# Optimization experiments

Hardware: AMD Instinct MI355X
Metric: run time of the kernel (lower is better)

Reference implementation:

```python
import jax, jax.numpy as jnp
import numpy as np

B, S, HID, NH, CACHE = 2, 1024, 1024, 16, 4096
HD = HID // NH
HOT = max(4, CACHE // 4)
COLD = CACHE - HOT
COMP = HID // 2
EPS = 1e-5


def setup_inputs() -> dict:
    key = jax.random.key(0)
    ks = jax.random.split(key, 16)
    std = 0.02
    inp = {
        'inputs': jax.random.normal(ks[0], (B, S, HID), jnp.float32),
        'hot_keys': std * jax.random.normal(ks[1], (HOT, HID), jnp.float32),
        'hot_values': std * jax.random.normal(ks[2], (HOT, HID), jnp.float32),
        'hot_age': jnp.zeros((HOT,), jnp.float32),
        'hot_access': jnp.zeros((HOT,), jnp.float32),
        'cold_keys': std * jax.random.normal(ks[3], (COLD, HID), jnp.float32),
        'cold_values': std * jax.random.normal(ks[4], (COLD, HID), jnp.float32),
        'cold_age': jnp.zeros((COLD,), jnp.float32),
        'cold_access': jnp.zeros((COLD,), jnp.float32),
        # linear weights stored [in, out] (y = x @ W + b)
        'Wq': std * jax.random.normal(ks[5], (HID, HID), jnp.float32),
        'bq': jnp.zeros((HID,), jnp.float32),
        'Wk': std * jax.random.normal(ks[6], (HID, HID), jnp.float32),
        'bk': jnp.zeros((HID,), jnp.float32),
        'Wv': std * jax.random.normal(ks[7], (HID, HID), jnp.float32),
        'bv': jnp.zeros((HID,), jnp.float32),
        'Wo': std * jax.random.normal(ks[8], (HID, HID), jnp.float32),
        'bo': jnp.zeros((HID,), jnp.float32),
        'Wc': (1.0 / np.sqrt(HID)) * jax.random.normal(ks[9], (HID, COMP), jnp.float32),
        'bc': jnp.zeros((COMP,), jnp.float32),
        'Wd': (1.0 / np.sqrt(COMP)) * jax.random.normal(ks[10], (COMP, HID), jnp.float32),
        'bd': jnp.zeros((HID,), jnp.float32),
        'gamma': jnp.ones((HID,), jnp.float32),
        'beta': jnp.zeros((HID,), jnp.float32),
    }
    return inp


def _cache_level(q, cache_k, v_flat, age, access, Wk, bk, Wo, bo):
    # q: [B, NH, S, HD]; cache_k/v_flat: [C, HID]
    C = cache_k.shape[0]
    k = (cache_k @ Wk + bk).reshape(C, NH, HD)
    v = v_flat.reshape(C, NH, HD)
    scores = jnp.einsum('bhsd,chd->bhsc', q, k) / np.sqrt(HD)
    scores = scores + (-0.1 * age + 0.05 * access)  # broadcast over [B,H,S,C]
    attn = jax.nn.softmax(scores, axis=-1)
    out = jnp.einsum('bhsc,chd->bhsd', attn, v)
    out = out.transpose(0, 2, 1, 3).reshape(q.shape[0], q.shape[2], HID)
    return out @ Wo + bo


def reference(inputs, hot_keys, hot_values, hot_age, hot_access,
              cold_keys, cold_values, cold_age, cold_access,
              Wq, bq, Wk, bk, Wv, bv, Wo, bo, Wc, bc, Wd, bd, gamma, beta):
    q = (inputs @ Wq + bq).reshape(B, S, NH, HD).transpose(0, 2, 1, 3)
    # hot tier: values through value_net
    hot_v = hot_values @ Wv + bv
    hot_out = _cache_level(q, hot_keys, hot_v, hot_age, hot_access, Wk, bk, Wo, bo)
    # cold tier: values through compressor -> decompressor
    cold_v = (cold_values @ Wc + bc) @ Wd + bd
    cold_out = _cache_level(q, cold_keys, cold_v, cold_age, cold_access, Wk, bk, Wo, bo)
    x = hot_out + cold_out
    mu = jnp.mean(x, axis=-1, keepdims=True)
    var = jnp.mean(jnp.square(x - mu), axis=-1, keepdims=True)
    return (x - mu) / jnp.sqrt(var + EPS) * gamma + beta
```

## Files before the change

kernel.cpp:

```cpp
#include <hip/hip_runtime.h>

#define BBATCH 2
#define SS   1024
#define HID  1024
#define NH   16
#define HD   64
#define HOT  1024
#define COLD 3072
#define COMP 512

typedef __attribute__((ext_vector_type(8))) short s8v;
typedef __attribute__((ext_vector_type(4))) float f4v;
typedef unsigned short u16;
typedef unsigned int   u32;

__device__ __forceinline__ float b2f(u16 u){ return __uint_as_float(((u32)u)<<16); }
__device__ __forceinline__ u16 f2b(float f){
  u32 u = __float_as_uint(f);
  u += 0x7FFF + ((u>>16)&1);
  return (u16)(u>>16);
}
__device__ __forceinline__ u32 pk2r(u32 a, u32 b){
  return __builtin_amdgcn_perm(b + 0x8000u, a + 0x8000u, 0x07060302u);
}
__device__ __forceinline__ float ldsc(const void* p, int i, int isf32){
  return isf32 ? ((const float*)p)[i] : b2f(((const u16*)p)[i]);
}
__device__ __forceinline__ void gl16(const u16* g, u16* l){
  __builtin_amdgcn_global_load_lds(
      (const __attribute__((address_space(1))) u32*)g,
      (__attribute__((address_space(3))) u32*)l, 16, 0, 0);
}

__global__ void detect_kernel(const u32* __restrict__ gamma_raw, u32* __restrict__ flag){
  if (threadIdx.x == 0) flag[0] = (gamma_raw[0] == 0x3F800000u) ? 1u : 0u;
}

__global__ __launch_bounds__(256) void bias_kernel(
    const void* __restrict__ h_age, const void* __restrict__ h_acc,
    const void* __restrict__ c_age, const void* __restrict__ c_acc,
    float* __restrict__ BiasH, float* __restrict__ BiasC, const u32* __restrict__ flag)
{
  const int f = (int)flag[0];
  const int i = blockIdx.x * 256 + threadIdx.x;
  if (i < HOT) BiasH[i] = -0.1f * ldsc(h_age, i, f) + 0.05f * ldsc(h_acc, i, f);
  const int j = i - HOT;
  if (j >= 0 && j < COLD) BiasC[j] = -0.1f * ldsc(c_age, j, f) + 0.05f * ldsc(c_acc, j, f);
}

struct CDesc { const void* S; u16* D; int tile0, pad; };
struct CBatch { CDesc d[5]; int nd; };

__global__ __launch_bounds__(256) void convert_multi(CBatch cb, const u32* __restrict__ flag)
{
  int di = 0;
  for (int i = 1; i < cb.nd; i++) if ((int)blockIdx.x >= cb.d[i].tile0) di = i;
  const CDesc g = cb.d[di];
  const int f = (int)flag[0];
  const size_t e0 = (size_t)(blockIdx.x - g.tile0) * 2048 + (size_t)threadIdx.x * 8;
  if (f) {
    const float* s = (const float*)g.S + e0;
    const uint4 x = *(const uint4*)s, y = *(const uint4*)(s + 4);
    *(uint4*)(g.D + e0) =
      (uint4){ pk2r(x.x,x.y), pk2r(x.z,x.w), pk2r(y.x,y.y), pk2r(y.z,y.w) };
  } else {
    *(uint4*)(g.D + e0) = *(const uint4*)((const u16*)g.S + e0);
  }
}

struct TDesc { const void* S; u16* D; int R, C, cshift, tile0; };
struct TBatch { TDesc d[6]; int nd; };

__global__ __launch_bounds__(256) void transpose_kernel(TBatch tb, const u32* __restrict__ flag)
{
  __shared__ __align__(16) u16 Tt[64][72];
  int di = 0;
  for (int i = 1; i < tb.nd; i++) if ((int)blockIdx.x >= tb.d[i].tile0) di = i;
  const TDesc g = tb.d[di];
  const int local = blockIdx.x - g.tile0;
  const int ty = local >> g.cshift;
  const int tx = local & ((1 << g.cshift) - 1);
  const int r0 = ty * 64, c0 = tx * 64;
  const int f = (int)flag[0];
  const int t = threadIdx.x;
  const int sr = t >> 2, sc = (t & 3) * 16;

  union { uint4 q[2]; u16 h[16]; } u;
  if (f) {
    const float* s = (const float*)g.S + (size_t)(r0 + sr) * g.C + c0 + sc;
    const uint4 a = *(const uint4*)s,     b = *(const uint4*)(s + 4);
    const uint4 c = *(const uint4*)(s + 8), d2 = *(const uint4*)(s + 12);
    u.q[0] = (uint4){ pk2r(a.x,a.y), pk2r(a.z,a.w), pk2r(b.x,b.y), pk2r(b.z,b.w) };
    u.q[1] = (uint4){ pk2r(c.x,c.y), pk2r(c.z,c.w), pk2r(d2.x,d2.y), pk2r(d2.z,d2.w) };
  } else {
    const u16* s = (const u16*)g.S + (size_t)(r0 + sr) * g.C + c0 + sc;
    u.q[0] = *(const uint4*)s;  u.q[1] = *(const uint4*)(s + 8);
  }
  #pragma unroll
  for (int i = 0; i < 16; i++) Tt[sc + i][sr] = u.h[i];
  __syncthreads();

  const int dc = t >> 2, dr = (t & 3) * 16;
  const uint4 o0 = *(const uint4*)&Tt[dc][dr];
  const uint4 o1 = *(const uint4*)&Tt[dc][dr + 8];
  u16* dp = g.D + (size_t)(c0 + dc) * g.R + r0 + dr;
  *(uint4*)dp = o0;  *(uint4*)(dp + 8) = o1;
}

#define BM 128
#define BN 64
#define BK 32
#define GSW(row, blk) (((row) << 5) + ((((blk) ^ (((row) >> 1) & 3))) << 3))

struct GemmDesc {
  const void* A; const u16* BT; const void* bias; u16* C;
  int aflag, bcol0, M, N, K, nxlog, tile0, ctrans;
  float bias_scale;
};
struct GemmBatch { GemmDesc d[6]; int nd; };

__global__ __launch_bounds__(256) void gemm_multi(GemmBatch bat, const u32* __restrict__ flag)
{
  __shared__ __align__(16) u16 As[BM * BK];
  __shared__ __align__(16) u16 Bs[BN * BK];

  int di = 0;
  for (int i = 1; i < bat.nd; i++) if ((int)blockIdx.x >= bat.d[i].tile0) di = i;
  const GemmDesc g = bat.d[di];
  const int local = blockIdx.x - g.tile0;
  const int ty = local >> g.nxlog;
  const int tx = local - (ty << g.nxlog);
  const int m0 = ty * BM, n0 = tx * BN;

  const int f  = (int)flag[0];
  const int af = g.aflag ? f : 0;

  const int tid  = threadIdx.x;
  const int lane = tid & 63, wave = tid >> 6;
  const int quad = lane >> 4, l15 = lane & 15;
  const int wy = wave >> 1, wx = wave & 1;

  f4v acc[4][2];
  #pragma unroll
  for (int i = 0; i < 4; i++)
    #pragma unroll
    for (int j = 0; j < 2; j++) acc[i][j] = (f4v){0.f,0.f,0.f,0.f};

  const int lrow = lane >> 2, lpos = lane & 3;
  const int arow0 = wave * 32 + lrow, arow1 = arow0 + 16;
  const int brow  = wave * 16 + lrow;
  const u16* gA0 = (const u16*)g.A + (size_t)(m0 + arow0) * g.K + ((lpos ^ ((arow0 >> 1) & 3)) << 3);
  const u16* gA1 = (const u16*)g.A + (size_t)(m0 + arow1) * g.K + ((lpos ^ ((arow1 >> 1) & 3)) << 3);
  const u16* gB0 = g.BT + (size_t)(g.bcol0 + n0 + brow) * g.K + ((lpos ^ ((brow >> 1) & 3)) << 3);
  u16* lA0 = &As[wave * 1024];
  u16* lA1 = &As[wave * 1024 + 512];
  u16* lB0 = &Bs[wave * 512];

  const int ar = tid >> 1, ac = (tid & 1) * 16;
  const int sAr = (ar >> 1) & 3, b0i = (tid & 1) * 2;
  uint4 a0, a1, a2, a3;
  auto load_Aregs = [&](int kk) {
    const float* s = (const float*)g.A + (size_t)(m0 + ar) * g.K + kk + ac;
    a0 = *(const uint4*)s;       a1 = *(const uint4*)(s + 4);
    a2 = *(const uint4*)(s + 8); a3 = *(const uint4*)(s + 12);
  };
  if (af) load_Aregs(0);

  for (int k0 = 0; k0 < g.K; k0 += BK) {
    __syncthreads();
    if (af) {
      *(uint4*)&As[(ar << 5) + (((b0i    ) ^ sAr) << 3)] =
        (uint4){ pk2r(a0.x,a0.y), pk2r(a0.z,a0.w), pk2r(a1.x,a1.y), pk2r(a1.z,a1.w) };
      *(uint4*)&As[(ar << 5) + (((b0i + 1) ^ sAr) << 3)] =
        (uint4){ pk2r(a2.x,a2.y), pk2r(a2.z,a2.w), pk2r(a3.x,a3.y), pk2r(a3.z,a3.w) };
    } else {
      gl16(gA0 + k0, lA0);
      gl16(gA1 + k0, lA1);
    }
    gl16(gB0 + k0, lB0);
    __syncthreads();

    if (af && k0 + BK < g.K) load_Aregs(k0 + BK);

    s8v afr[4], bfr[2];
    #pragma unroll
    for (int i = 0; i < 4; i++) {
      const int rr = wy * 64 + i * 16 + l15;
      afr[i] = *(const s8v*)&As[GSW(rr, quad)];
    }
    #pragma unroll
    for (int j = 0; j < 2; j++) {
      const int rb = wx * 32 + j * 16 + l15;
      bfr[j] = *(const s8v*)&Bs[GSW(rb, quad)];
    }

    #pragma unroll
    for (int j = 0; j < 2; j++)
      #pragma unroll
      for (int i = 0; i < 4; i++)
        acc[i][j] = __builtin_amdgcn_mfma_f32_16x16x32_bf16(afr[i], bfr[j], acc[i][j], 0, 0, 0);
  }

  if (g.ctrans) {
    #pragma unroll
    for (int j = 0; j < 2; j++) {
      const int col = n0 + wx * 32 + j * 16 + l15;
      const float bv = ldsc(g.bias, g.bcol0 + col, f) * g.bias_scale;
      #pragma unroll
      for (int i = 0; i < 4; i++) {
        const int row = m0 + wy * 64 + i * 16 + quad * 4;
        u16 t4[4];
        #pragma unroll
        for (int r = 0; r < 4; r++) t4[r] = f2b(acc[i][j][r] + bv);
        *(uint2*)&g.C[(size_t)col * g.M + row] = *(uint2*)t4;
      }
    }
  } else {
    #pragma unroll
    for (int j = 0; j < 2; j++) {
      const int col = n0 + wx * 32 + j * 16 + l15;
      const float bv = ldsc(g.bias, g.bcol0 + col, f) * g.bias_scale;
      #pragma unroll
      for (int i = 0; i < 4; i++) {
        const int row = m0 + wy * 64 + i * 16 + quad * 4;
        #pragma unroll
        for (int r = 0; r < 4; r++)
          g.C[(size_t)(row + r) * g.N + col] = f2b(acc[i][j][r] + bv);
      }
    }
  }
}

#define KV(row, blk) (((row) << 6) + ((((blk) ^ ((row) & 7))) << 3))

__global__ __launch_bounds__(256) void attn_kernel(
    const u16* __restrict__ Q,
    const u16* __restrict__ KHg, const u16* __restrict__ VHT,
    const u16* __restrict__ KCg, const u16* __restrict__ VCT,
    const float* __restrict__ BiasH, const float* __restrict__ BiasC,
    float* __restrict__ HotOut, float* __restrict__ ColdNum3, float* __restrict__ ColdZ3,
    int NG, int glog)
{
  __shared__ __align__(16) u16 Ks[64 * 64];
  __shared__ __align__(16) u16 Vs[64 * 64];

  const int tid  = threadIdx.x;
  const int lane = tid & 63, wave = tid >> 6;
  const int quad = lane >> 4, l15 = lane & 15;

  const int bx    = blockIdx.x;
  const int slice = bx & 3;
  const int sblk  = (bx >> 2) & 7;
  const int h     = (bx >> 5) & ((1 << glog) - 1);
  const int b     = bx >> (5 + glog);

  const int rowbase = b * SS + sblk * 128;
  const int hoff  = h * HD;
  const int myrow = wave * 32;

  const bool hot = (slice == 0);
  const u16*  Kt   = hot ? KHg : KCg;
  const u16*  Vt   = hot ? VHT : VCT;
  const float* Bias = hot ? BiasH : BiasC;
  const int   e0  = hot ? 0 : (slice - 1) * 1024;
  const int   ldv = hot ? HOT : COLD;

  const u16* qp = Q + (size_t)(rowbase + myrow + l15) * NG + hoff + quad * 8;
  const s8v aq0 = *(const s8v*)qp;
  const s8v aq1 = *(const s8v*)(qp + 32);
  const u16* qp1 = qp + (size_t)16 * NG;
  const s8v aq2 = *(const s8v*)qp1;
  const s8v aq3 = *(const s8v*)(qp1 + 32);

  const int rk = tid >> 2, cb2 = (tid & 3) * 2, sk = (tid & 3) * 16;
  const u16* kbase = Kt + (size_t)(e0 + rk) * NG + hoff + sk;
  const u16* vbase = Vt + (size_t)(hoff + rk) * ldv + e0 + sk;
  uint4 kr0 = *(const uint4*)kbase, kr1 = *(const uint4*)(kbase + 8);
  uint4 vr0 = *(const uint4*)vbase, vr1 = *(const uint4*)(vbase + 8);

  u16* kw0 = &Ks[KV(rk, cb2)];     u16* kw1 = &Ks[KV(rk, cb2 + 1)];
  u16* vw0 = &Vs[KV(rk, cb2)];     u16* vw1 = &Vs[KV(rk, cb2 + 1)];

  f4v o0[4], o1[4];
  #pragma unroll
  for (int j = 0; j < 4; j++) { o0[j] = (f4v){0.f,0.f,0.f,0.f}; o1[j] = (f4v){0.f,0.f,0.f,0.f}; }
  float zs0 = 0.f, zs1 = 0.f;

  for (int c0 = 0; c0 < 1024; c0 += 64) {
    __syncthreads();
    *(uint4*)kw0 = kr0;  *(uint4*)kw1 = kr1;
    *(uint4*)vw0 = vr0;  *(uint4*)vw1 = vr1;
    __syncthreads();
    if (c0 + 64 < 1024) {
      const u16* kn = kbase + (size_t)(c0 + 64) * NG;
      const u16* vn = vbase + (c0 + 64);
      kr0 = *(const uint4*)kn;  kr1 = *(const uint4*)(kn + 8);
      vr0 = *(const uint4*)vn;  vr1 = *(const uint4*)(vn + 8);
    }

    #pragma unroll
    for (int h2 = 0; h2 < 2; h2++) {
      const s8v ka0 = *(const s8v*)&Ks[KV(h2 * 32 + l15, quad)];
      const s8v ka1 = *(const s8v*)&Ks[KV(h2 * 32 + l15, 4 + quad)];
      const s8v kb0 = *(const s8v*)&Ks[KV(h2 * 32 + 16 + l15, quad)];
      const s8v kb1 = *(const s8v*)&Ks[KV(h2 * 32 + 16 + l15, 4 + quad)];

      const int cg0 = e0 + c0 + h2 * 32 + quad * 4;
      const float4 bi0 = *(const float4*)&Bias[cg0];
      const float4 bi1 = *(const float4*)&Bias[cg0 + 16];

      union { u32 w[4]; s8v v; } ap0, ap1;
      {
        f4v s0 = (f4v){0.f,0.f,0.f,0.f}, s1 = (f4v){0.f,0.f,0.f,0.f};
        s0 = __builtin_amdgcn_mfma_f32_16x16x32_bf16(ka0, aq0, s0, 0, 0, 0);
        s0 = __builtin_amdgcn_mfma_f32_16x16x32_bf16(ka1, aq1, s0, 0, 0, 0);
        s1 = __builtin_amdgcn_mfma_f32_16x16x32_bf16(kb0, aq0, s1, 0, 0, 0);
        s1 = __builtin_amdgcn_mfma_f32_16x16x32_bf16(kb1, aq1, s1, 0, 0, 0);
        float p0[4], p1[4];
        p0[0] = __expf(fminf(s0[0] * 0.125f + bi0.x, 30.f));
        p0[1] = __expf(fminf(s0[1] * 0.125f + bi0.y, 30.f));
        p0[2] = __expf(fminf(s0[2] * 0.125f + bi0.z, 30.f));
        p0[3] = __expf(fminf(s0[3] * 0.125f + bi0.w, 30.f));
        p1[0] = __expf(fminf(s1[0] * 0.125f + bi1.x, 30.f));
        p1[1] = __expf(fminf(s1[1] * 0.125f + bi1.y, 30.f));
        p1[2] = __expf(fminf(s1[2] * 0.125f + bi1.z, 30.f));
        p1[3] = __expf(fminf(s1[3] * 0.125f + bi1.w, 30.f));
        zs0 += p0[0] + p0[1] + p0[2] + p0[3] + p1[0] + p1[1] + p1[2] + p1[3];
        const u32 W0 = pk2r(__float_as_uint(p0[0]), __float_as_uint(p0[1]));
        const u32 W1 = pk2r(__float_as_uint(p0[2]), __float_as_uint(p0[3]));
        const u32 W2 = pk2r(__float_as_uint(p1[0]), __float_as_uint(p1[1]));
        const u32 W3 = pk2r(__float_as_uint(p1[2]), __float_as_uint(p1[3]));
        #pragma unroll
        for (int t = 0; t < 4; t++) {
          const int srcl = (((quad << 1) + (t >> 1)) & 3) * 16 + l15;
          const u32 lo = __shfl((t & 1) ? W1 : W0, srcl, 64);
          const u32 hi = __shfl((t & 1) ? W3 : W2, srcl, 64);
          ap0.w[t] = (quad >= 2) ? hi : lo;
        }
      }
      {
        f4v s0 = (f4v){0.f,0.f,0.f,0.f}, s1 = (f4v){0.f,0.f,0.f,0.f};
        s0 = __builtin_amdgcn_mfma_f32_16x16x32_bf16(ka0, aq2, s0, 0, 0, 0);
        s0 = __builtin_amdgcn_mfma_f32_16x16x32_bf16(ka1, aq3, s0, 0, 0, 0);
        s1 = __builtin_amdgcn_mfma_f32_16x16x32_bf16(kb0, aq2, s1, 0, 0, 0);
        s1 = __builtin_amdgcn_mfma_f32_16x16x32_bf16(kb1, aq3, s1, 0, 0, 0);
        float p0[4], p1[4];
        p0[0] = __expf(fminf(s0[0] * 0.125f + bi0.x, 30.f));
        p0[1] = __expf(fminf(s0[1] * 0.125f + bi0.y, 30.f));
        p0[2] = __expf(fminf(s0[2] * 0.125f + bi0.z, 30.f));
        p0[3] = __expf(fminf(s0[3] * 0.125f + bi0.w, 30.f));
        p1[0] = __expf(fminf(s1[0] * 0.125f + bi1.x, 30.f));
        p1[1] = __expf(fminf(s1[1] * 0.125f + bi1.y, 30.f));
        p1[2] = __expf(fminf(s1[2] * 0.125f + bi1.z, 30.f));
        p1[3] = __expf(fminf(s1[3] * 0.125f + bi1.w, 30.f));
        zs1 += p0[0] + p0[1] + p0[2] + p0[3] + p1[0] + p1[1] + p1[2] + p1[3];
        const u32 W0 = pk2r(__float_as_uint(p0[0]), __float_as_uint(p0[1]));
        const u32 W1 = pk2r(__float_as_uint(p0[2]), __float_as_uint(p0[3]));
        const u32 W2 = pk2r(__float_as_uint(p1[0]), __float_as_uint(p1[1]));
        const u32 W3 = pk2r(__float_as_uint(p1[2]), __float_as_uint(p1[3]));
        #pragma unroll
        for (int t = 0; t < 4; t++) {
          const int srcl = (((quad << 1) + (t >> 1)) & 3) * 16 + l15;
          const u32 lo = __shfl((t & 1) ? W1 : W0, srcl, 64);
          const u32 hi = __shfl((t & 1) ? W3 : W2, srcl, 64);
          ap1.w[t] = (quad >= 2) ? hi : lo;
        }
      }
      #pragma unroll
      for (int j2 = 0; j2 < 4; j2++) {
        const s8v bv = *(const s8v*)&Vs[KV(j2 * 16 + l15, h2 * 4 + quad)];
        o0[j2] = __builtin_amdgcn_mfma_f32_16x16x32_bf16(ap0.v, bv, o0[j2], 0, 0, 0);
        o1[j2] = __builtin_amdgcn_mfma_f32_16x16x32_bf16(ap1.v, bv, o1[j2], 0, 0, 0);
      }
    }
  }

  zs0 += __shfl_xor(zs0, 16, 64);  zs0 += __shfl_xor(zs0, 32, 64);
  zs1 += __shfl_xor(zs1, 16, 64);  zs1 += __shfl_xor(zs1, 32, 64);

  if (hot) {
    float rz0[4], rz1[4];
    #pragma unroll
    for (int r = 0; r < 4; r++) {
      rz0[r] = 1.0f / __shfl(zs0, quad * 4 + r, 64);
      rz1[r] = 1.0f / __shfl(zs1, quad * 4 + r, 64);
    }
    #pragma unroll
    for (int j = 0; j < 4; j++) {
      const int col = hoff + j * 16 + l15;
      #pragma unroll
      for (int r = 0; r < 4; r++) {
        const int row = rowbase + myrow + quad * 4 + r;
        HotOut[(size_t)row * NG + col]        = o0[j][r] * rz0[r];
        HotOut[(size_t)(row + 16) * NG + col] = o1[j][r] * rz1[r];
      }
    }
  } else {
    float* CN = ColdNum3 + (size_t)(slice - 1) * 2048 * NG;
    #pragma unroll
    for (int j = 0; j < 4; j++) {
      const int col = hoff + j * 16 + l15;
      #pragma unroll
      for (int r = 0; r < 4; r++) {
        const int row = rowbase + myrow + quad * 4 + r;
        CN[(size_t)row * NG + col]        = o0[j][r];
        CN[(size_t)(row + 16) * NG + col] = o1[j][r];
      }
    }
    if (lane < 16) {
      const size_t zb = (size_t)(slice - 1) * 2048 + rowbase + myrow;
      ColdZ3[(zb + lane) * (1 << glog) + h]      = zs0;
      ColdZ3[(zb + 16 + lane) * (1 << glog) + h] = zs1;
    }
  }
}

__global__ __launch_bounds__(256) void combine_kernel(
    const float* __restrict__ HotOut, const float* __restrict__ ColdNum3,
    const float* __restrict__ ColdZ3, u16* __restrict__ ATT,
    int att_ld, int att_c0, int NG, int glog)
{
  const int gid   = blockIdx.x * 256 + threadIdx.x;
  const int shift = 4 + glog;
  const int row   = gid >> shift;
  const int c4    = (gid & ((1 << shift) - 1)) << 2;
  const int h     = c4 >> 6;
  const int G     = 1 << glog;
  const size_t ps = (size_t)2048 * NG;
  const size_t zs = (size_t)2048 * G;

  const float4 hv = *(const float4*)&HotOut[(size_t)row * NG + c4];
  const float4 c1 = *(const float4*)&ColdNum3[(size_t)row * NG + c4];
  const float4 c2 = *(const float4*)&ColdNum3[ps + (size_t)row * NG + c4];
  const float4 c3 = *(const float4*)&ColdNum3[2 * ps + (size_t)row * NG + c4];
  const float z = ColdZ3[(size_t)row * G + h] + ColdZ3[zs + (size_t)row * G + h]
                + ColdZ3[2 * zs + (size_t)row * G + h];
  const float zi = 1.0f / z;

  u16 ov[4];
  ov[0] = f2b(hv.x + (c1.x + c2.x + c3.x) * zi);
  ov[1] = f2b(hv.y + (c1.y + c2.y + c3.y) * zi);
  ov[2] = f2b(hv.z + (c1.z + c2.z + c3.z) * zi);
  ov[3] = f2b(hv.w + (c1.w + c2.w + c3.w) * zi);
  *(uint2*)&ATT[(size_t)row * att_ld + att_c0 + c4] = *(uint2*)ov;
}

__global__ __launch_bounds__(256) void ln_kernel(
    const u16* __restrict__ X, const void* __restrict__ gamma,
    const void* __restrict__ beta, void* __restrict__ outp,
    const u32* __restrict__ flag)
{
  __shared__ float red[4];
  const int f = (int)flag[0];
  const int row = blockIdx.x, tid = threadIdx.x;
  const u16* xr = X + (size_t)row * HID;

  float x[4];
  { union { uint2 q; u16 hx[4]; } bx2;
    bx2.q = *(const uint2*)(xr + tid * 4);
    #pragma unroll
    for (int i = 0; i < 4; i++) x[i] = b2f(bx2.hx[i]); }

  float s = x[0] + x[1] + x[2] + x[3];
  #pragma unroll
  for (int m = 1; m < 64; m <<= 1) s += __shfl_xor(s, m, 64);
  if ((tid & 63) == 0) red[tid >> 6] = s;
  __syncthreads();
  const float mu = (red[0] + red[1] + red[2] + red[3]) * (1.0f / HID);
  __syncthreads();

  float v = 0.f;
  #pragma unroll
  for (int i = 0; i < 4; i++) { const float d = x[i] - mu; v += d * d; }
  #pragma unroll
  for (int m = 1; m < 64; m <<= 1) v += __shfl_xor(v, m, 64);
  if ((tid & 63) == 0) red[tid >> 6] = v;
  __syncthreads();
  const float var  = (red[0] + red[1] + red[2] + red[3]) * (1.0f / HID);
  const float rstd = 1.0f / sqrtf(var + 1e-5f);

  #pragma unroll
  for (int i = 0; i < 4; i++) {
    const int col = tid * 4 + i;
    const float val = (x[i] - mu) * rstd * ldsc(gamma, col, f) + ldsc(beta, col, f);
    if (f) ((float*)outp)[(size_t)row * HID + col] = val;
    else   ((u16*) outp)[(size_t)row * HID + col] = f2b(val);
  }
}

extern "C" void kernel_launch(void* const* d_in, const int* in_sizes, int n_in,
                              void* d_out, int out_size, void* d_ws, size_t ws_size,
                              hipStream_t stream)
{
  const void* inputs      = d_in[0];
  const void* hot_keys    = d_in[1];
  const void* hot_values  = d_in[2];
  const void* hot_age     = d_in[3];
  const void* hot_access  = d_in[4];
  const void* cold_keys   = d_in[5];
  const void* cold_values = d_in[6];
  const void* cold_age    = d_in[7];
  const void* cold_access = d_in[8];
  const void* Wq = d_in[9];   const void* bq = d_in[10];
  const void* Wk = d_in[11];  const void* bk = d_in[12];
  const void* Wv = d_in[13];  const void* bv = d_in[14];
  const void* Wo = d_in[15];  const void* bo = d_in[16];
  const void* Wc = d_in[17];  const void* bc = d_in[18];
  const void* Wd = d_in[19];  const void* bd = d_in[20];
  const void* gamma = d_in[21];
  const void* beta  = d_in[22];

  const size_t FIX    = 256 + 16384;
  const size_t WT     = (size_t)10 * 1024 * 1024;
  const size_t COPIES = (size_t)10240 * 1024 * 2;
  const size_t XB     = (size_t)2048 * HID * 2;
  auto PART = [](int Gc){ return (size_t)2048 * (64 * Gc) * 16 + (size_t)2048 * Gc * 12; };
  auto BUFS = [](int Gc){ return (size_t)10240 * (64 * Gc) * 2; };
  auto MX   = [](size_t a, size_t b){ return a > b ? a : b; };

  int G = 0, docopy = 0;
  { const size_t needF = FIX + WT + MX(COPIES, MX(PART(16), XB)) + BUFS(16);
    if (ws_size >= needF) { G = 16; docopy = 1; } }
  for (int c = 8; c >= 2 && !G; c >>= 1)
    if (ws_size >= FIX + WT + COPIES + MX(PART(c), XB) + BUFS(c)) { G = c; docopy = 1; }
  for (int c = 8; c >= 2 && !G; c >>= 1)
    if (ws_size >= FIX + WT + MX(PART(c), XB) + BUFS(c)) { G = c; docopy = 0; }
  if (!G) return;
  const int glog = (G == 16) ? 4 : (G == 8 ? 3 : (G == 4 ? 2 : 1));
  const int NG = 64 * G;
  const bool full = (G == 16);

  char* base  = (char*)d_ws;
  u32*  flag  = (u32*)base;
  float* BiasH = (float*)(base + 256);
  float* BiasC = BiasH + HOT;
  u16* WqT = (u16*)(base + FIX);
  u16* WkT = WqT + (size_t)1024 * 1024;
  u16* WvT = WkT + (size_t)1024 * 1024;
  u16* WoT = WvT + (size_t)1024 * 1024;
  u16* WcT = WoT + (size_t)1024 * 1024;
  u16* WdT = WcT + (size_t)512 * 1024;
  char* rp0 = base + FIX + WT;

  u16* inputsB = (u16*)rp0;
  u16* hotkB   = inputsB + (size_t)2048 * 1024;
  u16* coldkB  = hotkB   + (size_t)1024 * 1024;
  u16* hotvB   = coldkB  + (size_t)3072 * 1024;
  u16* coldvB  = hotvB   + (size_t)1024 * 1024;

  char* rp = rp0 + ((docopy && !full) ? COPIES : 0);
  u16*   X        = (u16*)rp;
  float* HotOut   = (float*)rp;
  float* ColdNum3 = (float*)(rp + (size_t)2048 * NG * 4);
  float* ColdZ3   = (float*)(rp + (size_t)2048 * NG * 16);
  const size_t Rbytes = full ? MX(COPIES, MX(PART(16), XB)) : MX(PART(G), XB);
  u16* Qg  = (u16*)(rp + Rbytes);
  u16* KHg = Qg  + (size_t)2048 * NG;
  u16* KCg = KHg + (size_t)HOT  * NG;
  u16* VHT = KCg + (size_t)COLD * NG;
  u16* VCT = VHT + (size_t)HOT  * NG;
  u16* ATT   = (u16*)d_out;
  u16* CVmid = (u16*)d_out + (size_t)2048 * 1024;

  const void* Aq = docopy ? (const void*)inputsB : inputs;
  const void* Ahk = docopy ? (const void*)hotkB  : hot_keys;
  const void* Ack = docopy ? (const void*)coldkB : cold_keys;
  const void* Ahv = docopy ? (const void*)hotvB  : hot_values;
  const void* Acv = docopy ? (const void*)coldvB : cold_values;
  const int afl = docopy ? 0 : 1;

  const dim3 blk(256);
  const int mQ = 2048 / BM, mH = HOT / BM, mC = COLD / BM;

  detect_kernel<<<dim3(1), dim3(64), 0, stream>>>((const u32*)gamma, flag);
  bias_kernel<<<dim3((HOT + COLD) / 256), blk, 0, stream>>>(
      hot_age, hot_access, cold_age, cold_access, BiasH, BiasC, flag);

  if (docopy) {
    CBatch cb; cb.nd = 5; int t = 0;
    cb.d[0] = { inputs,      inputsB, t, 0 }; t += 1024;
    cb.d[1] = { hot_keys,    hotkB,   t, 0 }; t += 512;
    cb.d[2] = { cold_keys,   coldkB,  t, 0 }; t += 1536;
    cb.d[3] = { hot_values,  hotvB,   t, 0 }; t += 512;
    cb.d[4] = { cold_values, coldvB,  t, 0 }; t += 1536;
    convert_multi<<<dim3(t), blk, 0, stream>>>(cb, flag);
  }
  { TBatch tb; tb.nd = 6; int t = 0;
    tb.d[0] = { Wq, WqT, 1024, 1024, 4, t }; t += 256;
    tb.d[1] = { Wk, WkT, 1024, 1024, 4, t }; t += 256;
    tb.d[2] = { Wv, WvT, 1024, 1024, 4, t }; t += 256;
    tb.d[3] = { Wo, WoT, 1024, 1024, 4, t }; t += 256;
    tb.d[4] = { Wc, WcT, 1024,  512, 3, t }; t += 128;
    tb.d[5] = { Wd, WdT,  512, 1024, 4, t }; t += 128;
    transpose_kernel<<<dim3(t), blk, 0, stream>>>(tb, flag);
  }

  if (full) {
    { GemmBatch bb; bb.nd = 5; int t = 0;
      bb.d[0] = { Aq,  WqT, bq, Qg,    afl, 0, 2048, 1024, 1024, 4, t, 0, 1.0f }; t += 16 * mQ;
      bb.d[1] = { Ahk, WkT, bk, KHg,   afl, 0, HOT,  1024, 1024, 4, t, 0, 1.0f }; t += 16 * mH;
      bb.d[2] = { Ack, WkT, bk, KCg,   afl, 0, COLD, 1024, 1024, 4, t, 0, 1.0f }; t += 16 * mC;
      bb.d[3] = { Ahv, WvT, bv, VHT,   afl, 0, HOT,  1024, 1024, 4, t, 1, 1.0f }; t += 16 * mH;
      bb.d[4] = { Acv, WcT, bc, CVmid, afl, 0, COLD,  512, 1024, 3, t, 0, 1.0f }; t += 8 * mC;
      gemm_multi<<<dim3(t), blk, 0, stream>>>(bb, flag);
    }
    { GemmBatch bb; bb.nd = 1;
      bb.d[0] = { CVmid, WdT, bd, VCT, 0, 0, COLD, 1024, 512, 4, 0, 1, 1.0f };
      gemm_multi<<<dim3(16 * mC), blk, 0, stream>>>(bb, flag);
    }
    attn_kernel<<<dim3(BBATCH * 16 * 8 * 4), blk, 0, stream>>>(
        Qg, KHg, VHT, KCg, VCT, BiasH, BiasC, HotOut, ColdNum3, ColdZ3, NG, glog);
    combine_kernel<<<dim3((2048 * (NG / 4)) / 256), blk, 0, stream>>>(
        HotOut, ColdNum3, ColdZ3, ATT, HID, 0, NG, glog);
  } else {
    { GemmBatch bb; bb.nd = 5; int t = 0;
      bb.d[0] = { Aq,  WqT, bq, Qg,    afl, 0, 2048, NG,  1024, glog, t, 0, 1.0f }; t += G * mQ;
      bb.d[1] = { Ahk, WkT, bk, KHg,   afl, 0, HOT,  NG,  1024, glog, t, 0, 1.0f }; t += G * mH;
      bb.d[2] = { Ack, WkT, bk, KCg,   afl, 0, COLD, NG,  1024, glog, t, 0, 1.0f }; t += G * mC;
      bb.d[3] = { Ahv, WvT, bv, VHT,   afl, 0, HOT,  NG,  1024, glog, t, 1, 1.0f }; t += G * mH;
      bb.d[4] = { Acv, WcT, bc, CVmid, afl, 0, COLD, 512, 1024, 3,    t, 0, 1.0f }; t += 8 * mC;
      gemm_multi<<<dim3(t), blk, 0, stream>>>(bb, flag);
    }
    { GemmBatch bb; bb.nd = 1;
      bb.d[0] = { CVmid, WdT, bd, VCT, 0, 0, COLD, NG, 512, glog, 0, 1, 1.0f };
      gemm_multi<<<dim3(G * mC), blk, 0, stream>>>(bb, flag);
    }
    attn_kernel<<<dim3(BBATCH * G * 8 * 4), blk, 0, stream>>>(
        Qg, KHg, VHT, KCg, VCT, BiasH, BiasC, HotOut, ColdNum3, ColdZ3, NG, glog);
    combine_kernel<<<dim3((2048 * (NG / 4)) / 256), blk, 0, stream>>>(
        HotOut, ColdNum3, ColdZ3, ATT, HID, 0, NG, glog);

    for (int p = 1; p < NH / G; ++p) {
      const int c0 = p * NG;
      GemmBatch bb; bb.nd = 5; int t = 0;
      bb.d[0] = { Aq,    WqT, bq, Qg,  afl, c0, 2048, NG, 1024, glog, t, 0, 1.0f }; t += G * mQ;
      bb.d[1] = { Ahk,   WkT, bk, KHg, afl, c0, HOT,  NG, 1024, glog, t, 0, 1.0f }; t += G * mH;
      bb.d[2] = { Ack,   WkT, bk, KCg, afl, c0, COLD, NG, 1024, glog, t, 0, 1.0f }; t += G * mC;
      bb.d[3] = { Ahv,   WvT, bv, VHT, afl, c0, HOT,  NG, 1024, glog, t, 1, 1.0f }; t += G * mH;
      bb.d[4] = { CVmid, WdT, bd, VCT, 0,   c0, COLD, NG, 512,  glog, t, 1, 1.0f }; t += G * mC;
      gemm_multi<<<dim3(t), blk, 0, stream>>>(bb, flag);

      attn_kernel<<<dim3(BBATCH * G * 8 * 4), blk, 0, stream>>>(
          Qg, KHg, VHT, KCg, VCT, BiasH, BiasC, HotOut, ColdNum3, ColdZ3, NG, glog);
      combine_kernel<<<dim3((2048 * (NG / 4)) / 256), blk, 0, stream>>>(
          HotOut, ColdNum3, ColdZ3, ATT, HID, c0, NG, glog);
    }
  }

  { GemmBatch bb; bb.nd = 1;
    bb.d[0] = { ATT, WoT, bo, X, 0, 0, 2048, 1024, 1024, 4, 0, 0, 2.0f };
    gemm_multi<<<dim3(16 * mQ), blk, 0, stream>>>(bb, flag);
  }
  ln_kernel<<<dim3(2048), blk, 0, stream>>>(X, gamma, beta, d_out, flag);
}
```

Before: 302.1 us.

## Fold compressor and decompressor weights into one product matrix

Precomputes Wc·Wd as a single 1024x1024 weight and folds bc·Wd+bd into one bias. The cold-value projection then becomes a single GEMM inside the batched projection launch, replacing the two chained GEMMs. This drops the separate second launch and the intermediate CVmid buffer. In exchange it adds a weight-product GEMM (1024x1024x512) on every call and a small bias kernel, and the cold-value GEMM now has K=1024 instead of the 512/1024 split, which can change rounding.

```diff
diff --git a/kernel.cpp b/kernel.cpp
--- a/kernel.cpp
+++ b/kernel.cpp
@@ -46,6 +46,19 @@
   if (i < HOT) BiasH[i] = -0.1f * ldsc(h_age, i, f) + 0.05f * ldsc(h_acc, i, f);
   const int j = i - HOT;
   if (j >= 0 && j < COLD) BiasC[j] = -0.1f * ldsc(c_age, j, f) + 0.05f * ldsc(c_acc, j, f);
+}
+
+__global__ __launch_bounds__(256) void bcd_kernel(
+    const void* __restrict__ Wd, const void* __restrict__ bc,
+    const void* __restrict__ bd, void* __restrict__ Bcd, const u32* __restrict__ flag)
+{
+  const int f = (int)flag[0];
+  const int n = blockIdx.x * 256 + threadIdx.x;
+  float acc = ldsc(bd, n, f);
+  for (int c = 0; c < COMP; c++)
+    acc += ldsc(bc, c, f) * ldsc(Wd, c * HID + n, f);
+  if (f) ((float*)Bcd)[n] = acc;
+  else   ((u16*) Bcd)[n] = f2b(acc);
 }
 
 struct CDesc { const void* S; u16* D; int tile0, pad; };
@@ -510,8 +523,8 @@
   const void* gamma = d_in[21];
   const void* beta  = d_in[22];
 
-  const size_t FIX    = 256 + 16384;
-  const size_t WT     = (size_t)10 * 1024 * 1024;
+  const size_t FIX    = 256 + 16384 + 4096;
+  const size_t WT     = (size_t)11 * 1024 * 1024;
   const size_t COPIES = (size_t)10240 * 1024 * 2;
   const size_t XB     = (size_t)2048 * HID * 2;
   auto PART = [](int Gc){ return (size_t)2048 * (64 * Gc) * 16 + (size_t)2048 * Gc * 12; };
@@ -534,12 +547,13 @@
   u32*  flag  = (u32*)base;
   float* BiasH = (float*)(base + 256);
   float* BiasC = BiasH + HOT;
-  u16* WqT = (u16*)(base + FIX);
-  u16* WkT = WqT + (size_t)1024 * 1024;
-  u16* WvT = WkT + (size_t)1024 * 1024;
-  u16* WoT = WvT + (size_t)1024 * 1024;
-  u16* WcT = WoT + (size_t)1024 * 1024;
-  u16* WdT = WcT + (size_t)512 * 1024;
+  void*  Bcd   = (void*)(base + 256 + 16384);
+  u16* WqT  = (u16*)(base + FIX);
+  u16* WkT  = WqT + (size_t)1024 * 1024;
+  u16* WvT  = WkT + (size_t)1024 * 1024;
+  u16* WoT  = WvT + (size_t)1024 * 1024;
+  u16* WdT  = WoT + (size_t)1024 * 1024;
+  u16* WcdT = WdT + (size_t)1024 * 512;
   char* rp0 = base + FIX + WT;
 
   u16* inputsB = (u16*)rp0;
@@ -559,8 +573,7 @@
   u16* KCg = KHg + (size_t)HOT  * NG;
   u16* VHT = KCg + (size_t)COLD * NG;
   u16* VCT = VHT + (size_t)HOT  * NG;
-  u16* ATT   = (u16*)d_out;
-  u16* CVmid = (u16*)d_out + (size_t)2048 * 1024;
+  u16* ATT = (u16*)d_out;
 
   const void* Aq = docopy ? (const void*)inputsB : inputs;
   const void* Ahk = docopy ? (const void*)hotkB  : hot_keys;
@@ -575,6 +588,7 @@
   detect_kernel<<<dim3(1), dim3(64), 0, stream>>>((const u32*)gamma, flag);
   bias_kernel<<<dim3((HOT + COLD) / 256), blk, 0, stream>>>(
       hot_age, hot_access, cold_age, cold_access, BiasH, BiasC, flag);
+  bcd_kernel<<<dim3(1024 / 256), blk, 0, stream>>>(Wd, bc, bd, Bcd, flag);
 
   if (docopy) {
     CBatch cb; cb.nd = 5; int t = 0;
@@ -585,59 +599,41 @@
     cb.d[4] = { cold_values, coldvB,  t, 0 }; t += 1536;
     convert_multi<<<dim3(t), blk, 0, stream>>>(cb, flag);
   }
-  { TBatch tb; tb.nd = 6; int t = 0;
+  { TBatch tb; tb.nd = 5; int t = 0;
     tb.d[0] = { Wq, WqT, 1024, 1024, 4, t }; t += 256;
     tb.d[1] = { Wk, WkT, 1024, 1024, 4, t }; t += 256;
     tb.d[2] = { Wv, WvT, 1024, 1024, 4, t }; t += 256;
     tb.d[3] = { Wo, WoT, 1024, 1024, 4, t }; t += 256;
-    tb.d[4] = { Wc, WcT, 1024,  512, 3, t }; t += 128;
-    tb.d[5] = { Wd, WdT,  512, 1024, 4, t }; t += 128;
+    tb.d[4] = { Wd, WdT,  512, 1024, 4, t }; t += 128;
     transpose_kernel<<<dim3(t), blk, 0, stream>>>(tb, flag);
+  }
+  { GemmBatch bb; bb.nd = 1;
+    bb.d[0] = { Wc, WdT, bq, WcdT, 1, 0, 1024, 1024, 512, 4, 0, 1, 0.0f };
+    gemm_multi<<<dim3(8 * 16), blk, 0, stream>>>(bb, flag);
   }
 
   if (full) {
     { GemmBatch bb; bb.nd = 5; int t = 0;
-      bb.d[0] = { Aq,  WqT, bq, Qg,    afl, 0, 2048, 1024, 1024, 4, t, 0, 1.0f }; t += 16 * mQ;
-      bb.d[1] = { Ahk, WkT, bk, KHg,   afl, 0, HOT,  1024, 1024, 4, t, 0, 1.0f }; t += 16 * mH;
-      bb.d[2] = { Ack, WkT, bk, KCg,   afl, 0, COLD, 1024, 1024, 4, t, 0, 1.0f }; t += 16 * mC;
-      bb.d[3] = { Ahv, WvT, bv, VHT,   afl, 0, HOT,  1024, 1024, 4, t, 1, 1.0f }; t += 16 * mH;
-      bb.d[4] = { Acv, WcT, bc, CVmid, afl, 0, COLD,  512, 1024, 3, t, 0, 1.0f }; t += 8 * mC;
+      bb.d[0] = { Aq,  WqT,  bq,  Qg,  afl, 0, 2048, 1024, 1024, 4, t, 0, 1.0f }; t += 16 * mQ;
+      bb.d[1] = { Ahk, WkT,  bk,  KHg, afl, 0, HOT,  1024, 1024, 4, t, 0, 1.0f }; t += 16 * mH;
+      bb.d[2] = { Ack, WkT,  bk,  KCg, afl, 0, COLD, 1024, 1024, 4, t, 0, 1.0f }; t += 16 * mC;
+      bb.d[3] = { Ahv, WvT,  bv,  VHT, afl, 0, HOT,  1024, 1024, 4, t, 1, 1.0f }; t += 16 * mH;
+      bb.d[4] = { Acv, WcdT, Bcd, VCT, afl, 0, COLD, 1024, 1024, 4, t, 1, 1.0f }; t += 16 * mC;
       gemm_multi<<<dim3(t), blk, 0, stream>>>(bb, flag);
-    }
-    { GemmBatch bb; bb.nd = 1;
-      bb.d[0] = { CVmid, WdT, bd, VCT, 0, 0, COLD, 1024, 512, 4, 0, 1, 1.0f };
-      gemm_multi<<<dim3(16 * mC), blk, 0, stream>>>(bb, flag);
     }
     attn_kernel<<<dim3(BBATCH * 16 * 8 * 4), blk, 0, stream>>>(
         Qg, KHg, VHT, KCg, VCT, BiasH, BiasC, HotOut, ColdNum3, ColdZ3, NG, glog);
     combine_kernel<<<dim3((2048 * (NG / 4)) / 256), blk, 0, stream>>>(
         HotOut, ColdNum3, ColdZ3, ATT, HID, 0, NG, glog);
   } else {
-    { GemmBatch bb; bb.nd = 5; int t = 0;
-      bb.d[0] = { Aq,  WqT, bq, Qg,    afl, 0, 2048, NG,  1024, glog, t, 0, 1.0f }; t += G * mQ;
-      bb.d[1] = { Ahk, WkT, bk, KHg,   afl, 0, HOT,  NG,  1024, glog, t, 0, 1.0f }; t += G * mH;
-      bb.d[2] = { Ack, WkT, bk, KCg,   afl, 0, COLD, NG,  1024, glog, t, 0, 1.0f }; t += G * mC;
-      bb.d[3] = { Ahv, WvT, bv, VHT,   afl, 0, HOT,  NG,  1024, glog, t, 1, 1.0f }; t += G * mH;
-      bb.d[4] = { Acv, WcT, bc, CVmid, afl, 0, COLD, 512, 1024, 3,    t, 0, 1.0f }; t += 8 * mC;
-      gemm_multi<<<dim3(t), blk, 0, stream>>>(bb, flag);
-    }
-    { GemmBatch bb; bb.nd = 1;
-      bb.d[0] = { CVmid, WdT, bd, VCT, 0, 0, COLD, NG, 512, glog, 0, 1, 1.0f };
-      gemm_multi<<<dim3(G * mC), blk, 0, stream>>>(bb, flag);
-    }
-    attn_kernel<<<dim3(BBATCH * G * 8 * 4), blk, 0, stream>>>(
-        Qg, KHg, VHT, KCg, VCT, BiasH, BiasC, HotOut, ColdNum3, ColdZ3, NG, glog);
-    combine_kernel<<<dim3((2048 * (NG / 4)) / 256), blk, 0, stream>>>(
-        HotOut, ColdNum3, ColdZ3, ATT, HID, 0, NG, glog);
-
-    for (int p = 1; p < NH / G; ++p) {
+    for (int p = 0; p < NH / G; ++p) {
       const int c0 = p * NG;
       GemmBatch bb; bb.nd = 5; int t = 0;
-      bb.d[0] = { Aq,    WqT, bq, Qg,  afl, c0, 2048, NG, 1024, glog, t, 0, 1.0f }; t += G * mQ;
-      bb.d[1] = { Ahk,   WkT, bk, KHg, afl, c0, HOT,  NG, 1024, glog, t, 0, 1.0f }; t += G * mH;
-      bb.d[2] = { Ack,   WkT, bk, KCg, afl, c0, COLD, NG, 1024, glog, t, 0, 1.0f }; t += G * mC;
-      bb.d[3] = { Ahv,   WvT, bv, VHT, afl, c0, HOT,  NG, 1024, glog, t, 1, 1.0f }; t += G * mH;
-      bb.d[4] = { CVmid, WdT, bd, VCT, 0,   c0, COLD, NG, 512,  glog, t, 1, 1.0f }; t += G * mC;
+      bb.d[0] = { Aq,  WqT,  bq,  Qg,  afl, c0, 2048, NG, 1024, glog, t, 0, 1.0f }; t += G * mQ;
+      bb.d[1] = { Ahk, WkT,  bk,  KHg, afl, c0, HOT,  NG, 1024, glog, t, 0, 1.0f }; t += G * mH;
+      bb.d[2] = { Ack, WkT,  bk,  KCg, afl, c0, COLD, NG, 1024, glog, t, 0, 1.0f }; t += G * mC;
+      bb.d[3] = { Ahv, WvT,  bv,  VHT, afl, c0, HOT,  NG, 1024, glog, t, 1, 1.0f }; t += G * mH;
+      bb.d[4] = { Acv, WcdT, Bcd, VCT, afl, c0, COLD, NG, 1024, glog, t, 1, 1.0f }; t += G * mC;
       gemm_multi<<<dim3(t), blk, 0, stream>>>(bb, flag);
 
       attn_kernel<<<dim3(BBATCH * G * 8 * 4), blk, 0, stream>>>(
```

Measured after the change: 381.2 us. 26.2% more time.
